# Kernel optimization log

Measured on AMD Instinct MI355X. Metric: run time of the kernel, lower is better.

## Reference

```python
import jax, jax.numpy as jnp
import numpy as np

N_HEAD = 16
D_HEAD = 64
ROPE_BASE = 10000.0


def rotate_half(x):
    # interleaved pair rotation: (x0,x1,x2,x3,...) -> (-x1,x0,-x3,x2,...)
    x1 = x[..., ::2]
    x2 = x[..., 1::2]
    return jnp.stack((-x2, x1), axis=-1).reshape(x.shape)


def rope_tables(T, d_head, dtype):
    inv_freq = 1.0 / (ROPE_BASE ** (jnp.arange(0, d_head, 2, dtype=jnp.float32) / d_head))
    t = jnp.arange(T, dtype=jnp.float32)
    freqs = jnp.outer(t, inv_freq)                       # [T, d_head/2]
    emb = jnp.repeat(freqs, 2, axis=-1)                  # [T, d_head]
    return jnp.cos(emb).astype(dtype), jnp.sin(emb).astype(dtype)


def setup_inputs() -> dict:
    key = jax.random.key(0)
    k1, k2, k3 = jax.random.split(key, 3)
    B, T, D = 4, 2048, 1024
    x = jax.random.normal(k1, (B, T, D), dtype=jnp.float32)
    W_attn = jax.random.normal(k2, (D, 3 * D), dtype=jnp.float32) * 0.02
    W_proj = jax.random.normal(k3, (D, D), dtype=jnp.float32) * 0.02
    return {"x": x, "W_attn": W_attn, "W_proj": W_proj}


def reference(x, W_attn, W_proj):
    B, T, D = x.shape
    qkv = x @ W_attn                                      # [B, T, 3D]
    qkv = qkv.reshape(B, T, 3, N_HEAD, D_HEAD).transpose(2, 0, 3, 1, 4)
    q, k, v = qkv[0], qkv[1], qkv[2]                      # [B, H, T, d]

    cos, sin = rope_tables(T, D_HEAD, q.dtype)            # [T, d]
    q = q * cos + rotate_half(q) * sin
    k = k * cos + rotate_half(k) * sin

    scale = 1.0 / jnp.sqrt(jnp.asarray(D_HEAD, dtype=q.dtype))
    att = jnp.einsum('bhqd,bhkd->bhqk', q, k) * scale     # [B, H, T, T]
    causal = jnp.tril(jnp.ones((T, T), dtype=bool))
    att = jnp.where(causal, att, jnp.asarray(-jnp.inf, dtype=att.dtype))
    att = jax.nn.softmax(att, axis=-1)
    y = jnp.einsum('bhqk,bhkd->bhqd', att, v)             # [B, H, T, d]
    y = y.transpose(0, 2, 1, 3).reshape(B, T, D)
    return y @ W_proj
```

## Files before the change

### kernel.cpp

```cpp
#include <hip/hip_runtime.h>
#include <hip/hip_bf16.h>

typedef unsigned short ushort_t;
typedef __attribute__((ext_vector_type(8))) short bf16x8;
typedef __attribute__((ext_vector_type(4))) float f32x4;
typedef __attribute__((ext_vector_type(4))) unsigned short u16x4;

#define DEVI __device__ __forceinline__

#define WAITVM(N) asm volatile("s_waitcnt vmcnt(" #N ")" ::: "memory")
DEVI void bar_raw() { asm volatile("s_barrier" ::: "memory"); }

DEVI ushort_t f2bf(float f) {
  __hip_bfloat16 h = __float2bfloat16(f);
  return __builtin_bit_cast(unsigned short, h);
}

typedef const __attribute__((address_space(1))) void gvoid_t;
typedef __attribute__((address_space(3))) void lvoid_t;

DEVI void gload_lds16(const void* g, void* l) {
  __builtin_amdgcn_global_load_lds((gvoid_t*)g, (lvoid_t*)l, 16, 0, 0);
}

DEVI f32x4 mfma16(bf16x8 a, bf16x8 b, f32x4 c) {
  return __builtin_amdgcn_mfma_f32_16x16x32_bf16(a, b, c, 0, 0, 0);
}

DEVI bf16x8 lds_frag(const ushort_t* base, int row, int k) {
  int ch = (k >> 3) ^ (row & 7);
  return *(const bf16x8*)(base + row * 64 + ch * 8);
}

template <int ROWS, int THR>
DEVI void stage_swz(const ushort_t* src, int ld, ushort_t* lds, int tid) {
#pragma unroll
  for (int i = 0; i < ROWS / (THR / 8); ++i) {
    int r = i * (THR / 8) + (tid >> 3);
    int p = tid & 7;
    int cl = p ^ (r & 7);
    gload_lds16(src + (size_t)r * ld + cl * 8, lds + r * 64 + p * 8);
  }
}


__global__ void k_convert(const float* __restrict__ in, ushort_t* __restrict__ out) {
  int i = blockIdx.x * 256 + threadIdx.x;
  float4 v = ((const float4*)in)[i];
  u16x4 o = {f2bf(v.x), f2bf(v.y), f2bf(v.z), f2bf(v.w)};
  ((u16x4*)out)[i] = o;
}

__global__ void k_transpose(const float* __restrict__ in, ushort_t* __restrict__ out,
                            int R, int C) {
  __shared__ ushort_t tile[64][65];
  int r0 = blockIdx.y * 64, c0 = blockIdx.x * 64;
  int t = threadIdx.x;
  int tc = t & 63, tr = t >> 6;
#pragma unroll
  for (int i = 0; i < 16; ++i) {
    int r = i * 4 + tr;
    tile[r][tc] = f2bf(in[(size_t)(r0 + r) * C + c0 + tc]);
  }
  __syncthreads();
#pragma unroll
  for (int i = 0; i < 16; ++i) {
    int c = i * 4 + tr;
    out[(size_t)(c0 + c) * R + r0 + tc] = tile[tc][c];
  }
}

__global__ void k_rope_tab(float* __restrict__ ct, float* __restrict__ st) {
  int idx = blockIdx.x * 256 + threadIdx.x;
  int t = idx >> 5, i = idx & 31;
  float inv = powf(10000.0f, -(float)(2 * i) * (1.0f / 64.0f));
  float fr = (float)t * inv;
  ct[idx] = cosf(fr);
  st[idx] = sinf(fr);
}


__global__ __launch_bounds__(256, 2) void k_gemm_qkv(
    const ushort_t* __restrict__ A, const ushort_t* __restrict__ Bt,
    const float* __restrict__ ct, const float* __restrict__ st,
    ushort_t* __restrict__ Qo, ushort_t* __restrict__ Ko, ushort_t* __restrict__ Vto) {
  __shared__ ushort_t sA[2][128 * 64];
  __shared__ ushort_t sB[2][128 * 64];
  int tid = threadIdx.x;
  int bid = blockIdx.x;
  int swz = (bid & 7) * 192 + (bid >> 3);
  int bm = swz / 24, bn = swz - bm * 24;
  int wid = tid >> 6, lane = tid & 63;
  int wm = wid >> 1, wn = wid & 1;
  const ushort_t* Abase = A + (size_t)bm * 128 * 1024;
  const ushort_t* Bbase = Bt + (size_t)bn * 128 * 1024;
  f32x4 acc[4][4] = {};
  stage_swz<128, 256>(Abase, 1024, sA[0], tid);
  stage_swz<128, 256>(Bbase, 1024, sB[0], tid);
  for (int kt = 0; kt < 16; ++kt) {
    int cur = kt & 1;
    if (kt < 15) {
      stage_swz<128, 256>(Abase + (kt + 1) * 64, 1024, sA[cur ^ 1], tid);
      stage_swz<128, 256>(Bbase + (kt + 1) * 64, 1024, sB[cur ^ 1], tid);
      WAITVM(8);
    } else {
      WAITVM(0);
    }
    bar_raw();
#pragma unroll
    for (int kk = 0; kk < 2; ++kk) {
      bf16x8 af[4], bfr[4];
#pragma unroll
      for (int mt = 0; mt < 4; ++mt)
        af[mt] = lds_frag(sA[cur], wm * 64 + mt * 16 + (lane & 15), kk * 32 + (lane >> 4) * 8);
#pragma unroll
      for (int nt = 0; nt < 4; ++nt)
        bfr[nt] = lds_frag(sB[cur], wn * 64 + nt * 16 + (lane & 15), kk * 32 + (lane >> 4) * 8);
#pragma unroll
      for (int mt = 0; mt < 4; ++mt)
#pragma unroll
        for (int nt = 0; nt < 4; ++nt) acc[mt][nt] = mfma16(af[mt], bfr[nt], acc[mt][nt]);
    }
    bar_raw();
  }
  int gm0 = bm * 128 + wm * 64;
  int gn0 = bn * 128 + wn * 64;
#pragma unroll
  for (int mt = 0; mt < 4; ++mt) {
#pragma unroll
    for (int nt = 0; nt < 4; ++nt) {
      f32x4 v = acc[mt][nt];
      int n = gn0 + nt * 16 + (lane & 15);
      int sidx = n >> 10, h = (n >> 6) & 15, d = n & 63;
      if (sidx == 2) {
        int m0r = gm0 + mt * 16 + (lane >> 4) * 4;
        int b = m0r >> 11, tpos = m0r & 2047;
        u16x4 pk = {f2bf(v[0]), f2bf(v[1]), f2bf(v[2]), f2bf(v[3])};
        *(u16x4*)(Vto + (((size_t)b * 16 + h) * 64 + d) * 2048 + tpos) = pk;
      } else {
        ushort_t* dst = (sidx == 0) ? Qo : Ko;
#pragma unroll
        for (int r = 0; r < 4; ++r) {
          float x = v[r];
          float px = __shfl_xor(x, 1);
          int m = gm0 + mt * 16 + (lane >> 4) * 4 + r;
          int b = m >> 11, tpos = m & 2047;
          float c = ct[tpos * 32 + (d >> 1)];
          float s = st[tpos * 32 + (d >> 1)];
          float val = (d & 1) ? (x * c + px * s) : (x * c - px * s);
          if (sidx == 0) val *= 0.18033688011112042f;
          dst[(((size_t)b * 16 + h) * 2048 + tpos) * 64 + d] = f2bf(val);
        }
      }
    }
  }
}


__global__ __launch_bounds__(256, 2) void k_attn(
    const ushort_t* __restrict__ Qg, const ushort_t* __restrict__ Kg,
    const ushort_t* __restrict__ Vtg, ushort_t* __restrict__ Yg) {
  __shared__ ushort_t sK[2][64 * 64];
  __shared__ ushort_t sV[2][64 * 64];
  __shared__ ushort_t sP[4][2][32 * 64];
  int bid = blockIdx.x;
  int tid = threadIdx.x;
  int wid = tid >> 6, lane = tid & 63;
  int bh = (bid & 7) * 8 + ((bid >> 3) & 7);
  int ps = bid >> 6;
  const ushort_t* Qb = Qg + (size_t)bh * (2048 * 64);
  const ushort_t* Kb = Kg + (size_t)bh * (2048 * 64);
  const ushort_t* Vb = Vtg + (size_t)bh * (64 * 2048);
  int b = bh >> 4, h = bh & 15;
  const bf16x8 ones = {0x3F80, 0x3F80, 0x3F80, 0x3F80, 0x3F80, 0x3F80, 0x3F80, 0x3F80};

  for (int t = 0; t < 2; ++t) {
    int qs = t ? (15 - ps) : ps;
    int q0 = qs * 128;
    int qw = q0 + wid * 32;
    int jmaxb = (q0 + 127) >> 6;
    int jmaxw = (qw + 31) >> 6;
    bf16x8 qf[2][2];
#pragma unroll
    for (int mt = 0; mt < 2; ++mt)
#pragma unroll
      for (int kk = 0; kk < 2; ++kk)
        qf[mt][kk] = *(const bf16x8*)(Qb + (size_t)(qw + mt * 16 + (lane & 15)) * 64 +
                                      kk * 32 + (lane >> 4) * 8);
    f32x4 o[2][4] = {};
    f32x4 l[2] = {};
    stage_swz<64, 256>(Kb, 64, sK[0], tid);
    stage_swz<64, 256>(Vb, 2048, sV[0], tid);
    for (int j = 0; j <= jmaxb; ++j) {
      int cur = j & 1;
      if (j < jmaxb) {
        stage_swz<64, 256>(Kb + (size_t)(j + 1) * 64 * 64, 64, sK[cur ^ 1], tid);
        stage_swz<64, 256>(Vb + (j + 1) * 64, 2048, sV[cur ^ 1], tid);
        WAITVM(4);
      } else {
        WAITVM(0);
      }
      bar_raw();
      if (j <= jmaxw) {
        ushort_t* sPw = sP[wid][cur];
        f32x4 st[2][4] = {};
        __builtin_amdgcn_s_setprio(1);
#pragma unroll
        for (int kk = 0; kk < 2; ++kk) {
          bf16x8 kf[4];
#pragma unroll
          for (int nt = 0; nt < 4; ++nt)
            kf[nt] = lds_frag(sK[cur], nt * 16 + (lane & 15), kk * 32 + (lane >> 4) * 8);
#pragma unroll
          for (int mt = 0; mt < 2; ++mt)
#pragma unroll
            for (int nt = 0; nt < 4; ++nt)
              st[mt][nt] = mfma16(kf[nt], qf[mt][kk], st[mt][nt]);
        }
        __builtin_amdgcn_s_setprio(0);
        if (j == jmaxw) {
#pragma unroll
          for (int mt = 0; mt < 2; ++mt)
#pragma unroll
            for (int nt = 0; nt < 4; ++nt)
#pragma unroll
              for (int r = 0; r < 4; ++r) {
                int kv = j * 64 + nt * 16 + (lane >> 4) * 4 + r;
                int q = qw + mt * 16 + (lane & 15);
                if (kv > q) st[mt][nt][r] = -1e30f;
              }
        }
        int g = lane >> 4;
#pragma unroll
        for (int mt = 0; mt < 2; ++mt) {
          int row = mt * 16 + (lane & 15);
#pragma unroll
          for (int nt = 0; nt < 4; ++nt) {
            u16x4 pk = {f2bf(__builtin_amdgcn_exp2f(st[mt][nt][0])),
                        f2bf(__builtin_amdgcn_exp2f(st[mt][nt][1])),
                        f2bf(__builtin_amdgcn_exp2f(st[mt][nt][2])),
                        f2bf(__builtin_amdgcn_exp2f(st[mt][nt][3]))};
            int ch = (nt * 2 + (g >> 1)) ^ (row & 7);
            *(u16x4*)(sPw + row * 64 + ch * 8 + (g & 1) * 4) = pk;
          }
        }
        __builtin_amdgcn_s_setprio(1);
#pragma unroll
        for (int kk = 0; kk < 2; ++kk) {
          bf16x8 pf[2], vf[4];
#pragma unroll
          for (int mt = 0; mt < 2; ++mt)
            pf[mt] = lds_frag(sPw, mt * 16 + (lane & 15), kk * 32 + (lane >> 4) * 8);
#pragma unroll
          for (int dt = 0; dt < 4; ++dt)
            vf[dt] = lds_frag(sV[cur], dt * 16 + (lane & 15), kk * 32 + (lane >> 4) * 8);
#pragma unroll
          for (int mt = 0; mt < 2; ++mt) {
#pragma unroll
            for (int dt = 0; dt < 4; ++dt) o[mt][dt] = mfma16(pf[mt], vf[dt], o[mt][dt]);
            l[mt] = mfma16(pf[mt], ones, l[mt]);
          }
        }
        __builtin_amdgcn_s_setprio(0);
      }
      bar_raw();
    }
#pragma unroll
    for (int mt = 0; mt < 2; ++mt)
#pragma unroll
      for (int r = 0; r < 4; ++r) {
        float inv = 1.0f / l[mt][r];
        int q = qw + mt * 16 + (lane >> 4) * 4 + r;
#pragma unroll
        for (int dt = 0; dt < 4; ++dt) {
          int d = dt * 16 + (lane & 15);
          Yg[((size_t)b * 2048 + q) * 1024 + h * 64 + d] = f2bf(o[mt][dt][r] * inv);
        }
      }
  }
}


__global__ __launch_bounds__(512, 2) void k_gemm_proj(
    const ushort_t* __restrict__ A, const ushort_t* __restrict__ Bt,
    float* __restrict__ out) {
  __shared__ ushort_t sA[2][256 * 64];
  __shared__ ushort_t sB[2][128 * 64];
  int tid = threadIdx.x;
  int bid = blockIdx.x;
  int swz = (bid & 7) * 32 + (bid >> 3);
  int bm = swz >> 3, bn = swz & 7;
  int lane = tid & 63;
  int wm = (tid >> 6) >> 2, wn = (tid >> 6) & 3;
  const ushort_t* Abase = A + (size_t)bm * 256 * 1024;
  const ushort_t* Bbase = Bt + (size_t)bn * 128 * 1024;
  f32x4 acc[8][2] = {};
  stage_swz<256, 512>(Abase, 1024, sA[0], tid);
  stage_swz<128, 512>(Bbase, 1024, sB[0], tid);
  for (int kt = 0; kt < 16; ++kt) {
    int cur = kt & 1;
    if (kt < 15) {
      stage_swz<256, 512>(Abase + (kt + 1) * 64, 1024, sA[cur ^ 1], tid);
      stage_swz<128, 512>(Bbase + (kt + 1) * 64, 1024, sB[cur ^ 1], tid);
      WAITVM(6);
    } else {
      WAITVM(0);
    }
    bar_raw();
#pragma unroll
    for (int kk = 0; kk < 2; ++kk) {
      bf16x8 af[8], bfr[2];
#pragma unroll
      for (int mt = 0; mt < 8; ++mt)
        af[mt] = lds_frag(sA[cur], wm * 128 + mt * 16 + (lane & 15), kk * 32 + (lane >> 4) * 8);
#pragma unroll
      for (int nt = 0; nt < 2; ++nt)
        bfr[nt] = lds_frag(sB[cur], wn * 32 + nt * 16 + (lane & 15), kk * 32 + (lane >> 4) * 8);
      __builtin_amdgcn_s_setprio(1);
#pragma unroll
      for (int mt = 0; mt < 8; ++mt)
#pragma unroll
        for (int nt = 0; nt < 2; ++nt) acc[mt][nt] = mfma16(af[mt], bfr[nt], acc[mt][nt]);
      __builtin_amdgcn_s_setprio(0);
    }
    bar_raw();
  }
  int gm0 = bm * 256 + wm * 128;
  int gn0 = bn * 128 + wn * 32;
#pragma unroll
  for (int mt = 0; mt < 8; ++mt)
#pragma unroll
    for (int nt = 0; nt < 2; ++nt) {
      f32x4 v = acc[mt][nt];
      int n = gn0 + nt * 16 + (lane & 15);
#pragma unroll
      for (int r = 0; r < 4; ++r) {
        int m = gm0 + mt * 16 + (lane >> 4) * 4 + r;
        out[(size_t)m * 1024 + n] = v[r];
      }
    }
}


extern "C" void kernel_launch(void* const* d_in, const int* in_sizes, int n_in,
                              void* d_out, int out_size, void* d_ws, size_t ws_size,
                              hipStream_t stream) {
  (void)in_sizes; (void)n_in; (void)out_size; (void)ws_size;
  const float* x  = (const float*)d_in[0];
  const float* Wa = (const float*)d_in[1];
  const float* Wp = (const float*)d_in[2];
  float* out = (float*)d_out;
  char* ws = (char*)d_ws;

  ushort_t* xb   = (ushort_t*)(ws + 0);
  ushort_t* WaT  = (ushort_t*)(ws + 16777216);
  ushort_t* WpT  = (ushort_t*)(ws + 23068672);
  float*    ctab = (float*)   (ws + 25165824);
  float*    stab = (float*)   (ws + 25427968);
  ushort_t* Qb   = (ushort_t*)(ws + 25690112);
  ushort_t* Kb   = (ushort_t*)(ws + 42467328);
  ushort_t* Vtb  = (ushort_t*)(ws + 59244544);

  k_convert<<<8192, 256, 0, stream>>>(x, xb);
  k_transpose<<<dim3(48, 16), 256, 0, stream>>>(Wa, WaT, 1024, 3072);
  k_transpose<<<dim3(16, 16), 256, 0, stream>>>(Wp, WpT, 1024, 1024);
  k_rope_tab<<<256, 256, 0, stream>>>(ctab, stab);
  k_gemm_qkv<<<1536, 256, 0, stream>>>(xb, WaT, ctab, stab, Qb, Kb, Vtb);
  k_attn<<<512, 256, 0, stream>>>(Qb, Kb, Vtb, xb);
  k_gemm_proj<<<256, 512, 0, stream>>>(xb, WpT, out);
}
```

Baseline: 163.2 us.

## Triple-buffer QKV GEMM with BK=32 stages and a single barrier per step

Reworks the QKV projection GEMM main loop from a double buffer with K-tile 64 and two barriers per step into a three-stage ring of K-tile 32. Loads are issued two tiles ahead right after one barrier, and MFMA blocks run at raised wave priority. The LDS footprint drops (48KB instead of 64KB), so launch bounds move to 3 blocks per CU to raise occupancy. The trade-off is twice as many loop iterations and barriers of smaller granularity, plus register pressure under the tighter launch bound.

Result: no change. 164.2 us (+0.6%).

```diff
diff --git a/kernel.cpp b/kernel.cpp
--- a/kernel.cpp
+++ b/kernel.cpp
@@ -9,6 +9,7 @@
 #define DEVI __device__ __forceinline__
 
 #define WAITVM(N) asm volatile("s_waitcnt vmcnt(" #N ")" ::: "memory")
+#define WAITLGKM0() asm volatile("s_waitcnt lgkmcnt(0)" ::: "memory")
 DEVI void bar_raw() { asm volatile("s_barrier" ::: "memory"); }
 
 DEVI ushort_t f2bf(float f) {
@@ -40,6 +41,21 @@
     int p = tid & 7;
     int cl = p ^ (r & 7);
     gload_lds16(src + (size_t)r * ld + cl * 8, lds + r * 64 + p * 8);
+  }
+}
+
+DEVI bf16x8 lds_frag32(const ushort_t* base, int row, int k) {
+  int ch = (k >> 3) ^ (row & 3);
+  return *(const bf16x8*)(base + row * 32 + ch * 8);
+}
+
+DEVI void stage32(const ushort_t* src, int ld, ushort_t* lds, int tid) {
+#pragma unroll
+  for (int i = 0; i < 2; ++i) {
+    int idx = i * 256 + tid;
+    int r = idx >> 2, p = idx & 3;
+    int cl = p ^ (r & 3);
+    gload_lds16(src + (size_t)r * ld + cl * 8, lds + idx * 8);
   }
 }
 
@@ -80,12 +96,12 @@
 }
 
 
-__global__ __launch_bounds__(256, 2) void k_gemm_qkv(
+__global__ __launch_bounds__(256, 3) void k_gemm_qkv(
     const ushort_t* __restrict__ A, const ushort_t* __restrict__ Bt,
     const float* __restrict__ ct, const float* __restrict__ st,
     ushort_t* __restrict__ Qo, ushort_t* __restrict__ Ko, ushort_t* __restrict__ Vto) {
-  __shared__ ushort_t sA[2][128 * 64];
-  __shared__ ushort_t sB[2][128 * 64];
+  __shared__ ushort_t sA[3][128 * 32];
+  __shared__ ushort_t sB[3][128 * 32];
   int tid = threadIdx.x;
   int bid = blockIdx.x;
   int swz = (bid & 7) * 192 + (bid >> 3);
@@ -95,34 +111,43 @@
   const ushort_t* Abase = A + (size_t)bm * 128 * 1024;
   const ushort_t* Bbase = Bt + (size_t)bn * 128 * 1024;
   f32x4 acc[4][4] = {};
-  stage_swz<128, 256>(Abase, 1024, sA[0], tid);
-  stage_swz<128, 256>(Bbase, 1024, sB[0], tid);
-  for (int kt = 0; kt < 16; ++kt) {
-    int cur = kt & 1;
-    if (kt < 15) {
-      stage_swz<128, 256>(Abase + (kt + 1) * 64, 1024, sA[cur ^ 1], tid);
-      stage_swz<128, 256>(Bbase + (kt + 1) * 64, 1024, sB[cur ^ 1], tid);
-      WAITVM(8);
+  int arow = wm * 64 + (lane & 15);
+  int brow = wn * 64 + (lane & 15);
+  int kcol = (lane >> 4) * 8;
+
+  stage32(Abase, 1024, sA[0], tid);
+  stage32(Bbase, 1024, sB[0], tid);
+  stage32(Abase + 32, 1024, sA[1], tid);
+  stage32(Bbase + 32, 1024, sB[1], tid);
+
+  int cb = 0, sb = 2;
+  for (int kt = 0; kt < 32; ++kt) {
+    WAITLGKM0();
+    if (kt <= 30) {
+      WAITVM(4);
     } else {
       WAITVM(0);
     }
     bar_raw();
-#pragma unroll
-    for (int kk = 0; kk < 2; ++kk) {
-      bf16x8 af[4], bfr[4];
-#pragma unroll
-      for (int mt = 0; mt < 4; ++mt)
-        af[mt] = lds_frag(sA[cur], wm * 64 + mt * 16 + (lane & 15), kk * 32 + (lane >> 4) * 8);
-#pragma unroll
-      for (int nt = 0; nt < 4; ++nt)
-        bfr[nt] = lds_frag(sB[cur], wn * 64 + nt * 16 + (lane & 15), kk * 32 + (lane >> 4) * 8);
-#pragma unroll
-      for (int mt = 0; mt < 4; ++mt)
-#pragma unroll
-        for (int nt = 0; nt < 4; ++nt) acc[mt][nt] = mfma16(af[mt], bfr[nt], acc[mt][nt]);
-    }
-    bar_raw();
-  }
+    if (kt < 30) {
+      stage32(Abase + (kt + 2) * 32, 1024, sA[sb], tid);
+      stage32(Bbase + (kt + 2) * 32, 1024, sB[sb], tid);
+    }
+    bf16x8 af[4], bfr[4];
+#pragma unroll
+    for (int mt = 0; mt < 4; ++mt) af[mt] = lds_frag32(sA[cb], arow + mt * 16, kcol);
+#pragma unroll
+    for (int nt = 0; nt < 4; ++nt) bfr[nt] = lds_frag32(sB[cb], brow + nt * 16, kcol);
+    __builtin_amdgcn_s_setprio(1);
+#pragma unroll
+    for (int mt = 0; mt < 4; ++mt)
+#pragma unroll
+      for (int nt = 0; nt < 4; ++nt) acc[mt][nt] = mfma16(af[mt], bfr[nt], acc[mt][nt]);
+    __builtin_amdgcn_s_setprio(0);
+    cb = (cb == 2) ? 0 : cb + 1;
+    sb = (sb == 2) ? 0 : sb + 1;
+  }
+
   int gm0 = bm * 128 + wm * 64;
   int gn0 = bn * 128 + wn * 64;
 #pragma unroll
```

## Enlarge QKV GEMM tile to 128x384 with 8 waves and interleaved staging

Applied to the files above, without the earlier changes.

Restructures the QKV projection GEMM from 128x128 tiles with 4 waves to 128x384 tiles with 8 waves (512 blocks of 512 threads). The K loop is split into four phases that interleave LDS fragment reads, next-tile global-to-LDS staging and MFMA bursts, with s_setprio raised around the MFMAs. The aim is more operand reuse per block and better overlap of memory and compute. In exchange LDS use grows to about 128 KB per block with one block per CU, and the loop adds more barriers.

Measured after the change: 162.5 us. About the same (-0.4%).

```diff
diff --git a/kernel.cpp b/kernel.cpp
--- a/kernel.cpp
+++ b/kernel.cpp
@@ -9,6 +9,7 @@
 #define DEVI __device__ __forceinline__
 
 #define WAITVM(N) asm volatile("s_waitcnt vmcnt(" #N ")" ::: "memory")
+#define WAITLGKM0() asm volatile("s_waitcnt lgkmcnt(0)" ::: "memory")
 DEVI void bar_raw() { asm volatile("s_barrier" ::: "memory"); }
 
 DEVI ushort_t f2bf(float f) {
@@ -80,57 +81,100 @@
 }
 
 
-__global__ __launch_bounds__(256, 2) void k_gemm_qkv(
+__global__ __launch_bounds__(512, 1) void k_gemm_qkv(
     const ushort_t* __restrict__ A, const ushort_t* __restrict__ Bt,
     const float* __restrict__ ct, const float* __restrict__ st,
     ushort_t* __restrict__ Qo, ushort_t* __restrict__ Ko, ushort_t* __restrict__ Vto) {
   __shared__ ushort_t sA[2][128 * 64];
-  __shared__ ushort_t sB[2][128 * 64];
+  __shared__ ushort_t sB[2][384 * 64];
   int tid = threadIdx.x;
   int bid = blockIdx.x;
-  int swz = (bid & 7) * 192 + (bid >> 3);
-  int bm = swz / 24, bn = swz - bm * 24;
+  int swz = (bid & 7) * 64 + (bid >> 3);
+  int bm = swz >> 3, bn = swz & 7;
   int wid = tid >> 6, lane = tid & 63;
-  int wm = wid >> 1, wn = wid & 1;
+  int wm = wid >> 2, wn = wid & 3;
+  int l15 = lane & 15, khi = (lane >> 4) * 8;
   const ushort_t* Abase = A + (size_t)bm * 128 * 1024;
-  const ushort_t* Bbase = Bt + (size_t)bn * 128 * 1024;
-  f32x4 acc[4][4] = {};
-  stage_swz<128, 256>(Abase, 1024, sA[0], tid);
-  stage_swz<128, 256>(Bbase, 1024, sB[0], tid);
-  for (int kt = 0; kt < 16; ++kt) {
-    int cur = kt & 1;
-    if (kt < 15) {
-      stage_swz<128, 256>(Abase + (kt + 1) * 64, 1024, sA[cur ^ 1], tid);
-      stage_swz<128, 256>(Bbase + (kt + 1) * 64, 1024, sB[cur ^ 1], tid);
-      WAITVM(8);
-    } else {
-      WAITVM(0);
-    }
-    bar_raw();
-#pragma unroll
-    for (int kk = 0; kk < 2; ++kk) {
-      bf16x8 af[4], bfr[4];
-#pragma unroll
-      for (int mt = 0; mt < 4; ++mt)
-        af[mt] = lds_frag(sA[cur], wm * 64 + mt * 16 + (lane & 15), kk * 32 + (lane >> 4) * 8);
-#pragma unroll
-      for (int nt = 0; nt < 4; ++nt)
-        bfr[nt] = lds_frag(sB[cur], wn * 64 + nt * 16 + (lane & 15), kk * 32 + (lane >> 4) * 8);
-#pragma unroll
-      for (int mt = 0; mt < 4; ++mt)
-#pragma unroll
-        for (int nt = 0; nt < 4; ++nt) acc[mt][nt] = mfma16(af[mt], bfr[nt], acc[mt][nt]);
-    }
-    bar_raw();
-  }
+  const ushort_t* Bbase = Bt + (size_t)bn * 384 * 1024;
+  f32x4 acc[4][6] = {};
+  int ar0 = wm * 64 + l15;
+  int br0 = wn * 96 + l15;
+
+  stage_swz<128, 512>(Abase, 1024, sA[0], tid);
+  stage_swz<384, 512>(Bbase, 1024, sB[0], tid);
+  WAITVM(0);
+  bar_raw();
+
+  for (int t = 0; t < 16; ++t) {
+    const ushort_t* sAt = sA[t & 1];
+    const ushort_t* sBt = sB[t & 1];
+    ushort_t* sAn = sA[(t + 1) & 1];
+    ushort_t* sBn = sB[(t + 1) & 1];
+    bf16x8 af[4], bf[3];
+#pragma unroll
+    for (int mt = 0; mt < 4; ++mt) af[mt] = lds_frag(sAt, ar0 + mt * 16, khi);
+#pragma unroll
+    for (int nt = 0; nt < 3; ++nt) bf[nt] = lds_frag(sBt, br0 + nt * 16, khi);
+    if (t < 15) stage_swz<128, 512>(Abase + (t + 1) * 64, 1024, sAn, tid);
+    bar_raw();
+    WAITLGKM0();
+    __builtin_amdgcn_s_setprio(1);
+#pragma unroll
+    for (int mt = 0; mt < 4; ++mt)
+#pragma unroll
+      for (int nt = 0; nt < 3; ++nt) acc[mt][nt] = mfma16(af[mt], bf[nt], acc[mt][nt]);
+    __builtin_amdgcn_s_setprio(0);
+    bar_raw();
+#pragma unroll
+    for (int nt = 0; nt < 3; ++nt) bf[nt] = lds_frag(sBt, br0 + 48 + nt * 16, khi);
+    if (t < 15) stage_swz<192, 512>(Bbase + (size_t)(t + 1) * 64, 1024, sBn, tid);
+    bar_raw();
+    WAITLGKM0();
+    __builtin_amdgcn_s_setprio(1);
+#pragma unroll
+    for (int mt = 0; mt < 4; ++mt)
+#pragma unroll
+      for (int nt = 0; nt < 3; ++nt) acc[mt][nt + 3] = mfma16(af[mt], bf[nt], acc[mt][nt + 3]);
+    __builtin_amdgcn_s_setprio(0);
+    bar_raw();
+#pragma unroll
+    for (int mt = 0; mt < 4; ++mt) af[mt] = lds_frag(sAt, ar0 + mt * 16, 32 + khi);
+#pragma unroll
+    for (int nt = 0; nt < 3; ++nt) bf[nt] = lds_frag(sBt, br0 + nt * 16, 32 + khi);
+    if (t < 15)
+      stage_swz<192, 512>(Bbase + (size_t)(t + 1) * 64 + 192 * 1024, 1024,
+                          sBn + 192 * 64, tid);
+    bar_raw();
+    WAITLGKM0();
+    __builtin_amdgcn_s_setprio(1);
+#pragma unroll
+    for (int mt = 0; mt < 4; ++mt)
+#pragma unroll
+      for (int nt = 0; nt < 3; ++nt) acc[mt][nt] = mfma16(af[mt], bf[nt], acc[mt][nt]);
+    __builtin_amdgcn_s_setprio(0);
+    bar_raw();
+#pragma unroll
+    for (int nt = 0; nt < 3; ++nt) bf[nt] = lds_frag(sBt, br0 + 48 + nt * 16, 32 + khi);
+    bar_raw();
+    WAITLGKM0();
+    __builtin_amdgcn_s_setprio(1);
+#pragma unroll
+    for (int mt = 0; mt < 4; ++mt)
+#pragma unroll
+      for (int nt = 0; nt < 3; ++nt) acc[mt][nt + 3] = mfma16(af[mt], bf[nt], acc[mt][nt + 3]);
+    __builtin_amdgcn_s_setprio(0);
+    if (t < 15) WAITVM(0);
+    bar_raw();
+  }
+
   int gm0 = bm * 128 + wm * 64;
-  int gn0 = bn * 128 + wn * 64;
+  int gn0 = bn * 384 + wn * 96;
 #pragma unroll
   for (int mt = 0; mt < 4; ++mt) {
 #pragma unroll
-    for (int nt = 0; nt < 4; ++nt) {
-      f32x4 v = acc[mt][nt];
-      int n = gn0 + nt * 16 + (lane & 15);
+    for (int j = 0; j < 6; ++j) {
+      f32x4 v = acc[mt][j];
+      int n = gn0 + j * 16 + l15;
       int sidx = n >> 10, h = (n >> 6) & 15, d = n & 63;
       if (sidx == 2) {
         int m0r = gm0 + mt * 16 + (lane >> 4) * 4;
@@ -365,7 +409,7 @@
   k_transpose<<<dim3(48, 16), 256, 0, stream>>>(Wa, WaT, 1024, 3072);
   k_transpose<<<dim3(16, 16), 256, 0, stream>>>(Wp, WpT, 1024, 1024);
   k_rope_tab<<<256, 256, 0, stream>>>(ctab, stab);
-  k_gemm_qkv<<<1536, 256, 0, stream>>>(xb, WaT, ctab, stab, Qb, Kb, Vtb);
+  k_gemm_qkv<<<512, 512, 0, stream>>>(xb, WaT, ctab, stab, Qb, Kb, Vtb);
   k_attn<<<512, 256, 0, stream>>>(Qb, Kb, Vtb, xb);
   k_gemm_proj<<<256, 512, 0, stream>>>(xb, WpT, out);
 }
```

## Widen QKV GEMM tile to 128x256 with triple-buffered LDS pipeline

Applied to the files above, without the earlier changes.

The QKV projection GEMM now uses 512-thread blocks computing 128x256 output tiles, with 8 waves arranged 2x4, and launches half as many blocks. LDS staging becomes a three-stage ring that prefetches two k-steps ahead. Each k-step is split into two halves so the A and B global loads for step t+2 are issued between fragment reads and MFMA bursts. MFMA sections also get raised wave priority. The aim is to hide global-load latency better and reuse each A tile across more columns, at the cost of more LDS per block, lower occupancy (one block per CU) and more barriers per step.

New measurement: 162.3 us. Within noise of the previous version (-0.6%).

```diff
diff --git a/kernel.cpp b/kernel.cpp
--- a/kernel.cpp
+++ b/kernel.cpp
@@ -9,6 +9,7 @@
 #define DEVI __device__ __forceinline__
 
 #define WAITVM(N) asm volatile("s_waitcnt vmcnt(" #N ")" ::: "memory")
+#define WAITLGKM0() asm volatile("s_waitcnt lgkmcnt(0)" ::: "memory")
 DEVI void bar_raw() { asm volatile("s_barrier" ::: "memory"); }
 
 DEVI ushort_t f2bf(float f) {
@@ -80,57 +81,84 @@
 }
 
 
-__global__ __launch_bounds__(256, 2) void k_gemm_qkv(
+__global__ __launch_bounds__(512, 1) void k_gemm_qkv(
     const ushort_t* __restrict__ A, const ushort_t* __restrict__ Bt,
     const float* __restrict__ ct, const float* __restrict__ st,
     ushort_t* __restrict__ Qo, ushort_t* __restrict__ Ko, ushort_t* __restrict__ Vto) {
-  __shared__ ushort_t sA[2][128 * 64];
-  __shared__ ushort_t sB[2][128 * 64];
+  __shared__ ushort_t sA[3][128 * 64];
+  __shared__ ushort_t sB[3][256 * 64];
   int tid = threadIdx.x;
   int bid = blockIdx.x;
-  int swz = (bid & 7) * 192 + (bid >> 3);
-  int bm = swz / 24, bn = swz - bm * 24;
+  int swz = (bid & 7) * 96 + (bid >> 3);
+  int bm = swz / 12, bn = swz % 12;
   int wid = tid >> 6, lane = tid & 63;
-  int wm = wid >> 1, wn = wid & 1;
+  int wm = wid >> 2, wn = wid & 3;
+  int l15 = lane & 15, khi = (lane >> 4) * 8;
   const ushort_t* Abase = A + (size_t)bm * 128 * 1024;
-  const ushort_t* Bbase = Bt + (size_t)bn * 128 * 1024;
+  const ushort_t* Bbase = Bt + (size_t)bn * 256 * 1024;
   f32x4 acc[4][4] = {};
-  stage_swz<128, 256>(Abase, 1024, sA[0], tid);
-  stage_swz<128, 256>(Bbase, 1024, sB[0], tid);
-  for (int kt = 0; kt < 16; ++kt) {
-    int cur = kt & 1;
-    if (kt < 15) {
-      stage_swz<128, 256>(Abase + (kt + 1) * 64, 1024, sA[cur ^ 1], tid);
-      stage_swz<128, 256>(Bbase + (kt + 1) * 64, 1024, sB[cur ^ 1], tid);
-      WAITVM(8);
-    } else {
+  int ar0 = wm * 64 + l15;
+  int br0 = wn * 64 + l15;
+
+  stage_swz<128, 512>(Abase, 1024, sA[0], tid);
+  stage_swz<256, 512>(Bbase, 1024, sB[0], tid);
+  stage_swz<128, 512>(Abase + 64, 1024, sA[1], tid);
+  stage_swz<256, 512>(Bbase + 64, 1024, sB[1], tid);
+  WAITVM(6);
+  bar_raw();
+
+  int cb = 0, sb = 2;
+  for (int t = 0; t < 16; ++t) {
+    const ushort_t* sAt = sA[cb];
+    const ushort_t* sBt = sB[cb];
+    bf16x8 af[4], bf[4];
+#pragma unroll
+    for (int mt = 0; mt < 4; ++mt) af[mt] = lds_frag(sAt, ar0 + mt * 16, khi);
+#pragma unroll
+    for (int nt = 0; nt < 4; ++nt) bf[nt] = lds_frag(sBt, br0 + nt * 16, khi);
+    if (t < 14) stage_swz<128, 512>(Abase + (t + 2) * 64, 1024, sA[sb], tid);
+    bar_raw();
+    WAITLGKM0();
+    __builtin_amdgcn_sched_barrier(0);
+    __builtin_amdgcn_s_setprio(1);
+#pragma unroll
+    for (int mt = 0; mt < 4; ++mt)
+#pragma unroll
+      for (int nt = 0; nt < 4; ++nt) acc[mt][nt] = mfma16(af[mt], bf[nt], acc[mt][nt]);
+    __builtin_amdgcn_s_setprio(0);
+    bar_raw();
+#pragma unroll
+    for (int mt = 0; mt < 4; ++mt) af[mt] = lds_frag(sAt, ar0 + mt * 16, 32 + khi);
+#pragma unroll
+    for (int nt = 0; nt < 4; ++nt) bf[nt] = lds_frag(sBt, br0 + nt * 16, 32 + khi);
+    if (t < 14) stage_swz<256, 512>(Bbase + (size_t)(t + 2) * 64, 1024, sB[sb], tid);
+    bar_raw();
+    WAITLGKM0();
+    __builtin_amdgcn_sched_barrier(0);
+    __builtin_amdgcn_s_setprio(1);
+#pragma unroll
+    for (int mt = 0; mt < 4; ++mt)
+#pragma unroll
+      for (int nt = 0; nt < 4; ++nt) acc[mt][nt] = mfma16(af[mt], bf[nt], acc[mt][nt]);
+    __builtin_amdgcn_s_setprio(0);
+    if (t < 14) {
+      WAITVM(6);
+    } else if (t == 14) {
       WAITVM(0);
     }
     bar_raw();
-#pragma unroll
-    for (int kk = 0; kk < 2; ++kk) {
-      bf16x8 af[4], bfr[4];
-#pragma unroll
-      for (int mt = 0; mt < 4; ++mt)
-        af[mt] = lds_frag(sA[cur], wm * 64 + mt * 16 + (lane & 15), kk * 32 + (lane >> 4) * 8);
-#pragma unroll
-      for (int nt = 0; nt < 4; ++nt)
-        bfr[nt] = lds_frag(sB[cur], wn * 64 + nt * 16 + (lane & 15), kk * 32 + (lane >> 4) * 8);
-#pragma unroll
-      for (int mt = 0; mt < 4; ++mt)
-#pragma unroll
-        for (int nt = 0; nt < 4; ++nt) acc[mt][nt] = mfma16(af[mt], bfr[nt], acc[mt][nt]);
-    }
-    bar_raw();
-  }
+    cb = (cb == 2) ? 0 : cb + 1;
+    sb = (sb == 2) ? 0 : sb + 1;
+  }
+
   int gm0 = bm * 128 + wm * 64;
-  int gn0 = bn * 128 + wn * 64;
+  int gn0 = bn * 256 + wn * 64;
 #pragma unroll
   for (int mt = 0; mt < 4; ++mt) {
 #pragma unroll
     for (int nt = 0; nt < 4; ++nt) {
       f32x4 v = acc[mt][nt];
-      int n = gn0 + nt * 16 + (lane & 15);
+      int n = gn0 + nt * 16 + l15;
       int sidx = n >> 10, h = (n >> 6) & 15, d = n & 63;
       if (sidx == 2) {
         int m0r = gm0 + mt * 16 + (lane >> 4) * 4;
@@ -365,7 +393,7 @@
   k_transpose<<<dim3(48, 16), 256, 0, stream>>>(Wa, WaT, 1024, 3072);
   k_transpose<<<dim3(16, 16), 256, 0, stream>>>(Wp, WpT, 1024, 1024);
   k_rope_tab<<<256, 256, 0, stream>>>(ctab, stab);
-  k_gemm_qkv<<<1536, 256, 0, stream>>>(xb, WaT, ctab, stab, Qb, Kb, Vtb);
+  k_gemm_qkv<<<768, 512, 0, stream>>>(xb, WaT, ctab, stab, Qb, Kb, Vtb);
   k_attn<<<512, 256, 0, stream>>>(Qb, Kb, Vtb, xb);
   k_gemm_proj<<<256, 512, 0, stream>>>(xb, WpT, out);
 }
```
